# Kernel tuning notes

Measured on AMD Instinct MI355X. Metric: run time of the kernel, lower is better.

The kernel has to match this reference:

```python
import jax, jax.numpy as jnp
import numpy as np

N_NODES = 50000
N_EDGES = 1600000
IN_CH = 512
HID_CH = 256


def _gcn_conv(x, edge_index, W, b):
    """PyG-style GCNConv: add self-loops, symmetric normalization, x@W then aggregate."""
    n = x.shape[0]
    loop = jnp.arange(n, dtype=edge_index.dtype)
    src = jnp.concatenate([edge_index[0], loop])  # [E+N]
    dst = jnp.concatenate([edge_index[1], loop])  # [E+N]
    deg = jax.ops.segment_sum(jnp.ones_like(dst, dtype=x.dtype), dst, num_segments=n)
    dinv = jnp.where(deg > 0, jax.lax.rsqrt(deg), 0.0)
    norm = dinv[src] * dinv[dst]  # [E+N]
    h = x @ W  # transform first (smaller feature dim for aggregation)
    msg = h[src] * norm[:, None]  # [E+N, F_out]
    out = jax.ops.segment_sum(msg, dst, num_segments=n)
    return out + b


def setup_inputs() -> dict:
    key = jax.random.key(0)
    ks = jax.random.split(key, 8)
    x = jax.random.normal(ks[0], (N_NODES, IN_CH), dtype=jnp.float32)
    edge_index = jax.random.randint(ks[1], (2, N_EDGES), 0, N_NODES, dtype=jnp.int32)
    W1 = jax.random.normal(ks[2], (IN_CH, HID_CH), dtype=jnp.float32) * (1.0 / np.sqrt(IN_CH))
    b1 = jnp.zeros((HID_CH,), dtype=jnp.float32)
    W2 = jax.random.normal(ks[3], (HID_CH, 32), dtype=jnp.float32) * (1.0 / np.sqrt(HID_CH))
    b2 = jnp.zeros((32,), dtype=jnp.float32)
    Wl = jax.random.normal(ks[4], (32, 2), dtype=jnp.float32) * (1.0 / np.sqrt(32))
    bl = jnp.zeros((2,), dtype=jnp.float32)
    return {"x": x, "edge_index": edge_index, "W1": W1, "b1": b1,
            "W2": W2, "b2": b2, "Wl": Wl, "bl": bl}


def reference(x, edge_index, W1, b1, W2, b2, Wl, bl):
    h = _gcn_conv(x, edge_index, W1, b1)
    h = jax.nn.relu(h)
    h = _gcn_conv(h, edge_index, W2, b2)
    # F.dropout(training=...) treated as identity (eval-mode reference)
    logits = h @ Wl + bl
    return jax.nn.log_softmax(logits, axis=1)
```

## Files before the change

### kernel.cpp

```cpp
#include <hip/hip_runtime.h>
#include <hip/hip_bf16.h>
#include <stdint.h>

#define NN 50000
#define NE 1600000
#define CIN 512
#define CH1 256
#define CH2 32

#define NBUCK 196
#define CAP 10240
#define ECH 4096
#define NCH 391

typedef __bf16 bf16_t;
typedef __attribute__((ext_vector_type(2))) __bf16 bf16x2;
typedef __attribute__((ext_vector_type(8))) __bf16 bf16x8;
typedef __attribute__((ext_vector_type(4))) float f32x4;

__device__ inline float blo(uint32_t v) { return __uint_as_float(v << 16); }
__device__ inline float bhi(uint32_t v) { return __uint_as_float(v & 0xffff0000u); }
__device__ inline uint32_t pk2(float a, float b) {
  bf16x2 p; p[0] = (__bf16)a; p[1] = (__bf16)b; return *(uint32_t*)&p;
}

__global__ __launch_bounds__(256) void k_hist(const int* __restrict__ dst,
                                              int* __restrict__ counts) {
  __shared__ int h[256];
  int blk = blockIdx.x, t = threadIdx.x;
  int e0 = blk * ECH;
  int ce = NE - e0; if (ce > ECH) ce = ECH;
  h[t] = 0;
  __syncthreads();
  for (int k = t; k < ce; k += 256) atomicAdd(&h[dst[e0 + k] >> 8], 1);
  __syncthreads();
  if (t < NBUCK) counts[blk * NBUCK + t] = h[t];
}

__global__ __launch_bounds__(512) void k_scanb(const int* __restrict__ counts,
                                               int* __restrict__ offs,
                                               int* __restrict__ bcnt) {
  __shared__ int l[512];
  int b = blockIdx.x, t = threadIdx.x;
  int v = (t < NCH) ? counts[t * NBUCK + b] : 0;
  int x = v;
  l[t] = x;
  __syncthreads();
  for (int off = 1; off < 512; off <<= 1) {
    int u = (t >= off) ? l[t - off] : 0;
    __syncthreads();
    x += u; l[t] = x;
    __syncthreads();
  }
  if (t < NCH) offs[t * NBUCK + b] = b * CAP + (x - v);
  if (t == 511) bcnt[b] = x;
}

__global__ __launch_bounds__(256) void k_bin(const int* __restrict__ src,
    const int* __restrict__ dst, const int* __restrict__ offs,
    uint32_t* __restrict__ binned) {
  __shared__ int h[256], lbase[256], lcnt[256], offsL[256];
  __shared__ uint32_t lstage[ECH];
  int blk = blockIdx.x, t = threadIdx.x;
  int e0 = blk * ECH;
  int ce = NE - e0; if (ce > ECH) ce = ECH;
  h[t] = 0; lcnt[t] = 0;
  if (t < NBUCK) offsL[t] = offs[blk * NBUCK + t];
  __syncthreads();
  for (int k = t; k < ce; k += 256) atomicAdd(&h[dst[e0 + k] >> 8], 1);
  __syncthreads();
  int v = h[t], x = v;
  lbase[t] = x;
  __syncthreads();
  for (int off = 1; off < 256; off <<= 1) {
    int u = (t >= off) ? lbase[t - off] : 0;
    __syncthreads();
    x += u; lbase[t] = x;
    __syncthreads();
  }
  lbase[t] = x - v;
  __syncthreads();
  for (int k = t; k < ce; k += 256) {
    int d = dst[e0 + k], s = src[e0 + k];
    int bkt = d >> 8;
    int p = lbase[bkt] + atomicAdd(&lcnt[bkt], 1);
    lstage[p] = ((uint32_t)bkt << 24) | ((uint32_t)(d & 255) << 16) | (uint32_t)s;
  }
  __syncthreads();
  for (int j = t; j < ce; j += 256) {
    uint32_t e = lstage[j];
    int bkt = e >> 24;
    binned[offsL[bkt] + (j - lbase[bkt])] = e & 0xffffffu >> 8 ? (e & 0x00ffffffu) : (e & 0x00ffffffu);
  }
}

__global__ __launch_bounds__(256) void k_build(const uint32_t* __restrict__ binned,
    const int* __restrict__ bcnt, int* __restrict__ rowptr, int* __restrict__ degg,
    float* __restrict__ dinv, int* __restrict__ csr) {
  __shared__ int hist[256], lrow[256], lcnt[256];
  __shared__ int csr_lds[CAP];
  int b = blockIdx.x, t = threadIdx.x;
  int count = bcnt[b];
  hist[t] = 0; lcnt[t] = 0;
  __syncthreads();
  const uint32_t* bb = binned + (size_t)b * CAP;
  for (int j = t; j < count; j += 256) atomicAdd(&hist[bb[j] >> 16], 1);
  __syncthreads();
  int v = hist[t], x = v;
  lrow[t] = x;
  __syncthreads();
  for (int off = 1; off < 256; off <<= 1) {
    int u = (t >= off) ? lrow[t - off] : 0;
    __syncthreads();
    x += u; lrow[t] = x;
    __syncthreads();
  }
  int excl = x - v;
  int node = b * 256 + t;
  if (node < NN) {
    rowptr[node] = b * CAP + excl;
    degg[node] = v;
    dinv[node] = 1.0f / sqrtf((float)(v + 1));
  }
  lrow[t] = excl;
  __syncthreads();
  for (int j = t; j < count; j += 256) {
    uint32_t e = bb[j];
    int dl = e >> 16;
    int p = lrow[dl] + atomicAdd(&lcnt[dl], 1);
    csr_lds[p] = (int)(e & 0xffffu);
  }
  __syncthreads();
  int* co = csr + (size_t)b * CAP;
  for (int j = t; j < count; j += 256) co[j] = csr_lds[j];
}

__global__ void k_prep_w(const float* __restrict__ W1, const float* __restrict__ W2,
                         bf16_t* __restrict__ w1t, bf16_t* __restrict__ w2t) {
  int i = blockIdx.x * 256 + threadIdx.x;
  if (i < CIN * CH1) {
    int n = i >> 9, k = i & 511;
    w1t[i] = (__bf16)W1[k * CH1 + n];
  }
  if (i < CH1 * CH2) {
    int oc = i >> 8, k = i & 255;
    w2t[i] = (__bf16)W2[k * CH2 + oc];
  }
}

#define BM 128
#define BN 128
#define BK 64

__global__ __launch_bounds__(256) void k_gemm1(const float* __restrict__ X,
                                               const bf16_t* __restrict__ BT,
                                               const float* __restrict__ dinv,
                                               bf16_t* __restrict__ h1b) {
  __shared__ __align__(16) bf16_t ldsA[2][BM * BK];
  __shared__ __align__(16) bf16_t ldsB[2][BN * BK];
  const int tid = threadIdx.x;
  const int lane = tid & 63;
  const int wid = tid >> 6;
  const int tm = blockIdx.x, tn = blockIdx.y;
  const int wm = wid >> 1, wn = wid & 1;

  f32x4 acc[4][4] = {};
  float4 ra[4], rb[4];

  auto loadA = [&](int kt) {
#pragma unroll
    for (int q = 0; q < 4; ++q) {
      int idx16 = q * 256 + tid;
      int r = idx16 >> 3, cw = idx16 & 7;
      int grow = tm * BM + r;
      grow = grow < NN ? grow : NN - 1;
      const float* ga = X + (size_t)grow * CIN + kt * BK + cw * 8;
      ra[q] = *(const float4*)ga;
      rb[q] = *(const float4*)(ga + 4);
    }
  };
  auto writeA = [&](int buf) {
#pragma unroll
    for (int q = 0; q < 4; ++q) {
      int idx16 = q * 256 + tid;
      int r = idx16 >> 3, cw = idx16 & 7;
      bf16x8 o;
      o[0] = (__bf16)ra[q].x; o[1] = (__bf16)ra[q].y;
      o[2] = (__bf16)ra[q].z; o[3] = (__bf16)ra[q].w;
      o[4] = (__bf16)rb[q].x; o[5] = (__bf16)rb[q].y;
      o[6] = (__bf16)rb[q].z; o[7] = (__bf16)rb[q].w;
      *(bf16x8*)&ldsA[buf][r * 64 + ((cw ^ (r & 7)) << 3)] = o;
    }
  };
  auto stageB = [&](int buf, int kt) {
#pragma unroll
    for (int t = 0; t < 4; ++t) {
      int o = t * 4096 + tid * 16;
      int r = o >> 7, cw = (o >> 4) & 7;
      int lc = cw ^ (r & 7);
      const bf16_t* gb = BT + (size_t)(tn * BN + r) * CIN + kt * BK + lc * 8;
      __builtin_amdgcn_global_load_lds(
          (const __attribute__((address_space(1))) void*)gb,
          (__attribute__((address_space(3))) void*)&ldsB[buf][(t * 4096 + wid * 1024) >> 1],
          16, 0, 0);
    }
  };

  loadA(0);
  stageB(0, 0);
  writeA(0);
  __syncthreads();
  int cur = 0;
  for (int kt = 0; kt < CIN / BK; ++kt) {
    if (kt + 1 < CIN / BK) { loadA(kt + 1); stageB(cur ^ 1, kt + 1); }
#pragma unroll
    for (int ks = 0; ks < 2; ++ks) {
      bf16x8 af[4], bfr[4];
#pragma unroll
      for (int m = 0; m < 4; ++m) {
        int row = wm * 64 + m * 16 + (lane & 15);
        int kc = ks * 4 + (lane >> 4);
        af[m] = *(const bf16x8*)&ldsA[cur][row * 64 + ((kc ^ (row & 7)) << 3)];
      }
#pragma unroll
      for (int n = 0; n < 4; ++n) {
        int col = wn * 64 + n * 16 + (lane & 15);
        int kc = ks * 4 + (lane >> 4);
        bfr[n] = *(const bf16x8*)&ldsB[cur][col * 64 + ((kc ^ (col & 7)) << 3)];
      }
#pragma unroll
      for (int m = 0; m < 4; ++m)
#pragma unroll
        for (int n = 0; n < 4; ++n)
          acc[m][n] = __builtin_amdgcn_mfma_f32_16x16x32_bf16(af[m], bfr[n], acc[m][n], 0, 0, 0);
    }
    if (kt + 1 < CIN / BK) writeA(cur ^ 1);
    __syncthreads();
    cur ^= 1;
  }

#pragma unroll
  for (int m = 0; m < 4; ++m) {
#pragma unroll
    for (int r = 0; r < 4; ++r) {
      int grow = tm * BM + wm * 64 + m * 16 + (lane >> 4) * 4 + r;
      if (grow < NN) {
        float dv = dinv[grow];
#pragma unroll
        for (int n = 0; n < 4; ++n) {
          int gcol = tn * BN + wn * 64 + n * 16 + (lane & 15);
          h1b[(size_t)grow * CH1 + gcol] = (__bf16)(dv * acc[m][n][r]);
        }
      }
    }
  }
}

#define ACC8(A, v) { A[0] += blo(v.x); A[1] += bhi(v.x); A[2] += blo(v.y); A[3] += bhi(v.y); \
                     A[4] += blo(v.z); A[5] += bhi(v.z); A[6] += blo(v.w); A[7] += bhi(v.w); }

__global__ __launch_bounds__(256) void k_agg1(const uint4* __restrict__ h1b,
    const int* __restrict__ rowptr, const int* __restrict__ degg,
    const int* __restrict__ csr, const float* __restrict__ dinv,
    const float* __restrict__ bias, uint4* __restrict__ hr) {
  const int i = blockIdx.x * 4 + (threadIdx.x >> 6);
  const int lane = threadIdx.x & 63;
  const int slot = lane & 31;
  const int grp = lane >> 5;

  float a[8] = {}, c[8] = {};
  if (grp == 0) {
    uint4 v = h1b[(size_t)i * 32 + slot];
    ACC8(a, v);
  }
  const int beg = rowptr[i], dg = degg[i];
  for (int base = 0; base < dg; base += 64) {
    int rem = dg - base;
    int cnt = rem > 64 ? 64 : rem;
    int idx = (lane < cnt) ? csr[beg + base + lane] : 0;
    int j = 0;
    for (; j + 4 <= cnt; j += 4) {
      int s0 = __shfl(idx, j + grp);
      int s1 = __shfl(idx, j + 2 + grp);
      uint4 v0 = h1b[(size_t)s0 * 32 + slot];
      uint4 v1 = h1b[(size_t)s1 * 32 + slot];
      ACC8(a, v0);
      ACC8(c, v1);
    }
    for (; j < cnt; j += 2) {
      int e = j + grp;
      int s = __shfl(idx, e < cnt ? e : 0);
      if (e < cnt) {
        uint4 v = h1b[(size_t)s * 32 + slot];
        ACC8(a, v);
      }
    }
  }
#pragma unroll
  for (int k = 0; k < 8; ++k) {
    a[k] += c[k];
    a[k] += __shfl_xor(a[k], 32);
  }
  if (grp == 0) {
    float di = dinv[i];
    float4 b0 = *(const float4*)&bias[slot * 8];
    float4 b1 = *(const float4*)&bias[slot * 8 + 4];
    float r0 = fmaxf(di * a[0] + b0.x, 0.f), r1 = fmaxf(di * a[1] + b0.y, 0.f);
    float r2 = fmaxf(di * a[2] + b0.z, 0.f), r3 = fmaxf(di * a[3] + b0.w, 0.f);
    float r4 = fmaxf(di * a[4] + b1.x, 0.f), r5 = fmaxf(di * a[5] + b1.y, 0.f);
    float r6 = fmaxf(di * a[6] + b1.z, 0.f), r7 = fmaxf(di * a[7] + b1.w, 0.f);
    uint4 o;
    o.x = pk2(r0, r1); o.y = pk2(r2, r3); o.z = pk2(r4, r5); o.w = pk2(r6, r7);
    hr[(size_t)i * 32 + slot] = o;
  }
}

__global__ __launch_bounds__(256) void k_gemm2(const bf16_t* __restrict__ hr,
    const bf16_t* __restrict__ w2t, const float* __restrict__ dinv,
    bf16_t* __restrict__ h2b) {
  const int lane = threadIdx.x & 63;
  const int gw = blockIdx.x * 4 + (threadIdx.x >> 6);
  const int r0 = gw * 16;
  if (r0 >= NN) return;
  int arow = r0 + (lane & 15);
  arow = arow < NN ? arow : NN - 1;
  const int kc = lane >> 4;
  f32x4 acc0 = {}, acc1 = {};
#pragma unroll
  for (int kb = 0; kb < 8; ++kb) {
    bf16x8 a  = *(const bf16x8*)&hr [(size_t)arow * CH1 + kb * 32 + kc * 8];
    bf16x8 b0 = *(const bf16x8*)&w2t[(size_t)(lane & 15) * CH1 + kb * 32 + kc * 8];
    bf16x8 b1 = *(const bf16x8*)&w2t[(size_t)(16 + (lane & 15)) * CH1 + kb * 32 + kc * 8];
    acc0 = __builtin_amdgcn_mfma_f32_16x16x32_bf16(a, b0, acc0, 0, 0, 0);
    acc1 = __builtin_amdgcn_mfma_f32_16x16x32_bf16(a, b1, acc1, 0, 0, 0);
  }
#pragma unroll
  for (int r = 0; r < 4; ++r) {
    int rr = r0 + (lane >> 4) * 4 + r;
    if (rr < NN) {
      float dv = dinv[rr];
      h2b[(size_t)rr * CH2 + (lane & 15)]      = (__bf16)(dv * acc0[r]);
      h2b[(size_t)rr * CH2 + 16 + (lane & 15)] = (__bf16)(dv * acc1[r]);
    }
  }
}

__global__ __launch_bounds__(256) void k_agg2(const uint2* __restrict__ h2b,
    const int* __restrict__ rowptr, const int* __restrict__ degg,
    const int* __restrict__ csr, const float* __restrict__ dinv,
    const float* __restrict__ b2, const float* __restrict__ Wl,
    const float* __restrict__ bl, float* __restrict__ out) {
  const int i = blockIdx.x * 4 + (threadIdx.x >> 6);
  const int lane = threadIdx.x & 63;
  const int s = lane & 7;
  const int g = lane >> 3;

  float a[4] = {};
  if (g == 0) {
    uint2 v = h2b[(size_t)i * 8 + s];
    a[0] += blo(v.x); a[1] += bhi(v.x); a[2] += blo(v.y); a[3] += bhi(v.y);
  }
  const int beg = rowptr[i], dg = degg[i];
  for (int base = 0; base < dg; base += 64) {
    int rem = dg - base;
    int cnt = rem > 64 ? 64 : rem;
    int idx = (lane < cnt) ? csr[beg + base + lane] : 0;
    int j = 0;
    for (; j + 8 <= cnt; j += 8) {
      int sr = __shfl(idx, j + g);
      uint2 v = h2b[(size_t)sr * 8 + s];
      a[0] += blo(v.x); a[1] += bhi(v.x); a[2] += blo(v.y); a[3] += bhi(v.y);
    }
    if (j < cnt) {
      int e = j + g;
      int sr = __shfl(idx, e < cnt ? e : 0);
      if (e < cnt) {
        uint2 v = h2b[(size_t)sr * 8 + s];
        a[0] += blo(v.x); a[1] += bhi(v.x); a[2] += blo(v.y); a[3] += bhi(v.y);
      }
    }
  }
#pragma unroll
  for (int k = 0; k < 4; ++k) {
    a[k] += __shfl_xor(a[k], 8);
    a[k] += __shfl_xor(a[k], 16);
    a[k] += __shfl_xor(a[k], 32);
  }
  float di = dinv[i];
  float4 bb = *(const float4*)&b2[s * 4];
  float v0 = di * a[0] + bb.x, v1 = di * a[1] + bb.y;
  float v2 = di * a[2] + bb.z, v3 = di * a[3] + bb.w;
  float2 w0 = *(const float2*)&Wl[(s * 4 + 0) * 2];
  float2 w1 = *(const float2*)&Wl[(s * 4 + 1) * 2];
  float2 w2 = *(const float2*)&Wl[(s * 4 + 2) * 2];
  float2 w3 = *(const float2*)&Wl[(s * 4 + 3) * 2];
  float l0 = v0 * w0.x + v1 * w1.x + v2 * w2.x + v3 * w3.x;
  float l1 = v0 * w0.y + v1 * w1.y + v2 * w2.y + v3 * w3.y;
#pragma unroll
  for (int off = 1; off < 8; off <<= 1) {
    l0 += __shfl_xor(l0, off);
    l1 += __shfl_xor(l1, off);
  }
  if (lane == 0) {
    l0 += bl[0]; l1 += bl[1];
    float m = fmaxf(l0, l1);
    float lse = m + logf(expf(l0 - m) + expf(l1 - m));
    float2 o; o.x = l0 - lse; o.y = l1 - lse;
    *(float2*)&out[i * 2] = o;
  }
}

extern "C" void kernel_launch(void* const* d_in, const int* in_sizes, int n_in,
                              void* d_out, int out_size, void* d_ws, size_t ws_size,
                              hipStream_t stream) {
  const float* x  = (const float*)d_in[0];
  const int*   ei = (const int*)d_in[1];
  const float* W1 = (const float*)d_in[2];
  const float* b1 = (const float*)d_in[3];
  const float* W2 = (const float*)d_in[4];
  const float* b2 = (const float*)d_in[5];
  const float* Wl = (const float*)d_in[6];
  const float* bl = (const float*)d_in[7];
  float* out = (float*)d_out;

  const int* src = ei;
  const int* dst = ei + NE;

  uint8_t* w = (uint8_t*)d_ws;
  auto alloc = [&](size_t bytes) { void* p = w; w += (bytes + 255) & ~(size_t)255; return p; };
  int*      counts = (int*)alloc((size_t)NCH * NBUCK * 4);
  int*      offs   = (int*)alloc((size_t)NCH * NBUCK * 4);
  int*      bcnt   = (int*)alloc((size_t)NBUCK * 4);
  uint32_t* binned = (uint32_t*)alloc((size_t)NBUCK * CAP * 4);
  int*      csr    = (int*)alloc((size_t)NBUCK * CAP * 4);
  int*      rowptr = (int*)alloc((size_t)NN * 4);
  int*      degg   = (int*)alloc((size_t)NN * 4);
  float*    dinv   = (float*)alloc((size_t)NN * 4);
  bf16_t*   w1t    = (bf16_t*)alloc((size_t)CIN * CH1 * 2);
  bf16_t*   w2t    = (bf16_t*)alloc((size_t)CH1 * CH2 * 2);
  bf16_t*   h1b    = (bf16_t*)alloc((size_t)NN * CH1 * 2);
  bf16_t*   hr     = (bf16_t*)alloc((size_t)NN * CH1 * 2);
  bf16_t*   h2b    = (bf16_t*)alloc((size_t)NN * CH2 * 2);

  k_hist <<<NCH, 256, 0, stream>>>(dst, counts);
  k_scanb<<<NBUCK, 512, 0, stream>>>(counts, offs, bcnt);
  k_bin  <<<NCH, 256, 0, stream>>>(src, dst, offs, binned);
  k_build<<<NBUCK, 256, 0, stream>>>(binned, bcnt, rowptr, degg, dinv, csr);

  k_prep_w<<<(CIN * CH1 + 255) / 256, 256, 0, stream>>>(W1, W2, w1t, w2t);

  dim3 g1((NN + BM - 1) / BM, CH1 / BN);
  k_gemm1<<<g1, 256, 0, stream>>>(x, w1t, dinv, h1b);

  k_agg1<<<NN / 4, 256, 0, stream>>>((const uint4*)h1b, rowptr, degg, csr, dinv, b1,
                                     (uint4*)hr);
  k_gemm2<<<(NN / 16 + 3) / 4, 256, 0, stream>>>(hr, w2t, dinv, h2b);
  k_agg2<<<NN / 4, 256, 0, stream>>>((const uint2*)h2b, rowptr, degg, csr, dinv,
                                     b2, Wl, bl, out);
}
```

Before: 243.7 us.

## Split hidden features into 32-column planes for cache-local aggregation

```diff
diff --git a/kernel.cpp b/kernel.cpp
--- a/kernel.cpp
+++ b/kernel.cpp
@@ -17,6 +17,7 @@
 typedef __attribute__((ext_vector_type(2))) __bf16 bf16x2;
 typedef __attribute__((ext_vector_type(8))) __bf16 bf16x8;
 typedef __attribute__((ext_vector_type(4))) float f32x4;
+typedef __attribute__((ext_vector_type(2))) uint32_t u32x2;
 
 __device__ inline float blo(uint32_t v) { return __uint_as_float(v << 16); }
 __device__ inline float bhi(uint32_t v) { return __uint_as_float(v & 0xffff0000u); }
@@ -90,7 +91,7 @@
   for (int j = t; j < ce; j += 256) {
     uint32_t e = lstage[j];
     int bkt = e >> 24;
-    binned[offsL[bkt] + (j - lbase[bkt])] = e & 0xffffffu >> 8 ? (e & 0x00ffffffu) : (e & 0x00ffffffu);
+    binned[offsL[bkt] + (j - lbase[bkt])] = e & 0x00ffffffu;
   }
 }
 
@@ -155,7 +156,7 @@
 __global__ __launch_bounds__(256) void k_gemm1(const float* __restrict__ X,
                                                const bf16_t* __restrict__ BT,
                                                const float* __restrict__ dinv,
-                                               bf16_t* __restrict__ h1b) {
+                                               bf16_t* __restrict__ h1p) {
   __shared__ __align__(16) bf16_t ldsA[2][BM * BK];
   __shared__ __align__(16) bf16_t ldsB[2][BN * BK];
   const int tid = threadIdx.x;
@@ -249,73 +250,77 @@
 #pragma unroll
         for (int n = 0; n < 4; ++n) {
           int gcol = tn * BN + wn * 64 + n * 16 + (lane & 15);
-          h1b[(size_t)grow * CH1 + gcol] = (__bf16)(dv * acc[m][n][r]);
+          int plane = gcol >> 5, pc = gcol & 31;
+          h1p[(size_t)plane * (NN * 32) + (size_t)grow * 32 + pc] =
+              (__bf16)(dv * acc[m][n][r]);
         }
       }
     }
   }
 }
 
-#define ACC8(A, v) { A[0] += blo(v.x); A[1] += bhi(v.x); A[2] += blo(v.y); A[3] += bhi(v.y); \
-                     A[4] += blo(v.z); A[5] += bhi(v.z); A[6] += blo(v.w); A[7] += bhi(v.w); }
-
-__global__ __launch_bounds__(256) void k_agg1(const uint4* __restrict__ h1b,
+__global__ __launch_bounds__(256) void k_agg1(const u32x2* __restrict__ h1p,
     const int* __restrict__ rowptr, const int* __restrict__ degg,
     const int* __restrict__ csr, const float* __restrict__ dinv,
-    const float* __restrict__ bias, uint4* __restrict__ hr) {
-  const int i = blockIdx.x * 4 + (threadIdx.x >> 6);
+    const float* __restrict__ bias, u32x2* __restrict__ hrp) {
+  const int s = blockIdx.x & 7;
+  const int i = (blockIdx.x >> 3) * 4 + (threadIdx.x >> 6);
   const int lane = threadIdx.x & 63;
-  const int slot = lane & 31;
-  const int grp = lane >> 5;
-
-  float a[8] = {}, c[8] = {};
-  if (grp == 0) {
-    uint4 v = h1b[(size_t)i * 32 + slot];
-    ACC8(a, v);
-  }
-  const int beg = rowptr[i], dg = degg[i];
+  const int q = lane & 7;
+  const int g = lane >> 3;
+
+  const u32x2* P = h1p + (size_t)s * (NN * 8);
+
+  float a0 = 0.f, a1 = 0.f, a2 = 0.f, a3 = 0.f;
+  float c0 = 0.f, c1 = 0.f, c2 = 0.f, c3 = 0.f;
+  if (g == 0) {
+    u32x2 v = P[(size_t)i * 8 + q];
+    a0 = blo(v.x); a1 = bhi(v.x); a2 = blo(v.y); a3 = bhi(v.y);
+  }
+  const int beg = __builtin_nontemporal_load(&rowptr[i]);
+  const int dg  = __builtin_nontemporal_load(&degg[i]);
   for (int base = 0; base < dg; base += 64) {
-    int rem = dg - base;
-    int cnt = rem > 64 ? 64 : rem;
-    int idx = (lane < cnt) ? csr[beg + base + lane] : 0;
+    int cnt = dg - base; if (cnt > 64) cnt = 64;
+    int idx = (lane < cnt) ? __builtin_nontemporal_load(&csr[beg + base + lane]) : 0;
     int j = 0;
-    for (; j + 4 <= cnt; j += 4) {
-      int s0 = __shfl(idx, j + grp);
-      int s1 = __shfl(idx, j + 2 + grp);
-      uint4 v0 = h1b[(size_t)s0 * 32 + slot];
-      uint4 v1 = h1b[(size_t)s1 * 32 + slot];
-      ACC8(a, v0);
-      ACC8(c, v1);
-    }
-    for (; j < cnt; j += 2) {
-      int e = j + grp;
-      int s = __shfl(idx, e < cnt ? e : 0);
+    for (; j + 16 <= cnt; j += 16) {
+      int s0 = __shfl(idx, j + g);
+      int s1 = __shfl(idx, j + 8 + g);
+      u32x2 v0 = P[(size_t)s0 * 8 + q];
+      u32x2 v1 = P[(size_t)s1 * 8 + q];
+      a0 += blo(v0.x); a1 += bhi(v0.x); a2 += blo(v0.y); a3 += bhi(v0.y);
+      c0 += blo(v1.x); c1 += bhi(v1.x); c2 += blo(v1.y); c3 += bhi(v1.y);
+    }
+    for (; j < cnt; j += 8) {
+      int e = j + g;
+      int sm = __shfl(idx, e < cnt ? e : 0);
       if (e < cnt) {
-        uint4 v = h1b[(size_t)s * 32 + slot];
-        ACC8(a, v);
+        u32x2 v = P[(size_t)sm * 8 + q];
+        a0 += blo(v.x); a1 += bhi(v.x); a2 += blo(v.y); a3 += bhi(v.y);
       }
     }
   }
-#pragma unroll
-  for (int k = 0; k < 8; ++k) {
-    a[k] += c[k];
-    a[k] += __shfl_xor(a[k], 32);
-  }
-  if (grp == 0) {
+  a0 += c0; a1 += c1; a2 += c2; a3 += c3;
+#pragma unroll
+  for (int off = 8; off < 64; off <<= 1) {
+    a0 += __shfl_xor(a0, off);
+    a1 += __shfl_xor(a1, off);
+    a2 += __shfl_xor(a2, off);
+    a3 += __shfl_xor(a3, off);
+  }
+  if (g == 0) {
     float di = dinv[i];
-    float4 b0 = *(const float4*)&bias[slot * 8];
-    float4 b1 = *(const float4*)&bias[slot * 8 + 4];
-    float r0 = fmaxf(di * a[0] + b0.x, 0.f), r1 = fmaxf(di * a[1] + b0.y, 0.f);
-    float r2 = fmaxf(di * a[2] + b0.z, 0.f), r3 = fmaxf(di * a[3] + b0.w, 0.f);
-    float r4 = fmaxf(di * a[4] + b1.x, 0.f), r5 = fmaxf(di * a[5] + b1.y, 0.f);
-    float r6 = fmaxf(di * a[6] + b1.z, 0.f), r7 = fmaxf(di * a[7] + b1.w, 0.f);
-    uint4 o;
-    o.x = pk2(r0, r1); o.y = pk2(r2, r3); o.z = pk2(r4, r5); o.w = pk2(r6, r7);
-    hr[(size_t)i * 32 + slot] = o;
-  }
-}
-
-__global__ __launch_bounds__(256) void k_gemm2(const bf16_t* __restrict__ hr,
+    float4 bb = *(const float4*)&bias[s * 32 + q * 4];
+    float r0 = fmaxf(di * a0 + bb.x, 0.f);
+    float r1 = fmaxf(di * a1 + bb.y, 0.f);
+    float r2 = fmaxf(di * a2 + bb.z, 0.f);
+    float r3 = fmaxf(di * a3 + bb.w, 0.f);
+    u32x2 o; o.x = pk2(r0, r1); o.y = pk2(r2, r3);
+    __builtin_nontemporal_store(o, &hrp[((size_t)s * NN + i) * 8 + q]);
+  }
+}
+
+__global__ __launch_bounds__(256) void k_gemm2(const bf16_t* __restrict__ hrp,
     const bf16_t* __restrict__ w2t, const float* __restrict__ dinv,
     bf16_t* __restrict__ h2b) {
   const int lane = threadIdx.x & 63;
@@ -328,7 +333,7 @@
   f32x4 acc0 = {}, acc1 = {};
 #pragma unroll
   for (int kb = 0; kb < 8; ++kb) {
-    bf16x8 a  = *(const bf16x8*)&hr [(size_t)arow * CH1 + kb * 32 + kc * 8];
+    bf16x8 a  = *(const bf16x8*)&hrp[(size_t)kb * (NN * 32) + (size_t)arow * 32 + kc * 8];
     bf16x8 b0 = *(const bf16x8*)&w2t[(size_t)(lane & 15) * CH1 + kb * 32 + kc * 8];
     bf16x8 b1 = *(const bf16x8*)&w2t[(size_t)(16 + (lane & 15)) * CH1 + kb * 32 + kc * 8];
     acc0 = __builtin_amdgcn_mfma_f32_16x16x32_bf16(a, b0, acc0, 0, 0, 0);
@@ -360,11 +365,11 @@
     uint2 v = h2b[(size_t)i * 8 + s];
     a[0] += blo(v.x); a[1] += bhi(v.x); a[2] += blo(v.y); a[3] += bhi(v.y);
   }
-  const int beg = rowptr[i], dg = degg[i];
+  const int beg = __builtin_nontemporal_load(&rowptr[i]);
+  const int dg  = __builtin_nontemporal_load(&degg[i]);
   for (int base = 0; base < dg; base += 64) {
-    int rem = dg - base;
-    int cnt = rem > 64 ? 64 : rem;
-    int idx = (lane < cnt) ? csr[beg + base + lane] : 0;
+    int cnt = dg - base; if (cnt > 64) cnt = 64;
+    int idx = (lane < cnt) ? __builtin_nontemporal_load(&csr[beg + base + lane]) : 0;
     int j = 0;
     for (; j + 8 <= cnt; j += 8) {
       int sr = __shfl(idx, j + g);
@@ -438,8 +443,8 @@
   float*    dinv   = (float*)alloc((size_t)NN * 4);
   bf16_t*   w1t    = (bf16_t*)alloc((size_t)CIN * CH1 * 2);
   bf16_t*   w2t    = (bf16_t*)alloc((size_t)CH1 * CH2 * 2);
-  bf16_t*   h1b    = (bf16_t*)alloc((size_t)NN * CH1 * 2);
-  bf16_t*   hr     = (bf16_t*)alloc((size_t)NN * CH1 * 2);
+  bf16_t*   h1p    = (bf16_t*)alloc((size_t)NN * CH1 * 2);
+  bf16_t*   hrp    = (bf16_t*)alloc((size_t)NN * CH1 * 2);
   bf16_t*   h2b    = (bf16_t*)alloc((size_t)NN * CH2 * 2);
 
   k_hist <<<NCH, 256, 0, stream>>>(dst, counts);
@@ -450,11 +455,11 @@
   k_prep_w<<<(CIN * CH1 + 255) / 256, 256, 0, stream>>>(W1, W2, w1t, w2t);
 
   dim3 g1((NN + BM - 1) / BM, CH1 / BN);
-  k_gemm1<<<g1, 256, 0, stream>>>(x, w1t, dinv, h1b);
-
-  k_agg1<<<NN / 4, 256, 0, stream>>>((const uint4*)h1b, rowptr, degg, csr, dinv, b1,
-                                     (uint4*)hr);
-  k_gemm2<<<(NN / 16 + 3) / 4, 256, 0, stream>>>(hr, w2t, dinv, h2b);
+  k_gemm1<<<g1, 256, 0, stream>>>(x, w1t, dinv, h1p);
+
+  k_agg1<<<(NN / 4) * 8, 256, 0, stream>>>((const u32x2*)h1p, rowptr, degg, csr,
+                                           dinv, b1, (u32x2*)hrp);
+  k_gemm2<<<(NN / 16 + 3) / 4, 256, 0, stream>>>(hrp, w2t, dinv, h2b);
   k_agg2<<<NN / 4, 256, 0, stream>>>((const uint2*)h2b, rowptr, degg, csr, dinv,
                                      b2, Wl, bl, out);
 }
```

Result: slower. 343.7 us (+41.1%).
